# Performance work log

Measured on AMD Instinct MI355X. Metric: run time of the kernel, lower is better.

The kernel has to match this reference:

```python
import jax, jax.numpy as jnp
import numpy as np

B, T, C = 2, 2048, 2048
H, KH, D = 16, 4, 128
EPS = 1e-6

def _rmsnorm(x, w, eps=EPS):
    # norm over last dim in fp32, matching torch RMSNorm
    xf = x.astype(jnp.float32)
    var = jnp.mean(xf * xf, axis=-1, keepdims=True)
    return w * (xf * jax.lax.rsqrt(var + eps)).astype(x.dtype)

def _rotate_half(x):
    x1, x2 = jnp.split(x, 2, axis=-1)
    return jnp.concatenate((-x2, x1), axis=-1)

def setup_inputs() -> dict:
    key = jax.random.key(0)
    ks = jax.random.split(key, 9)
    s = 0.02
    return {
        "x": jax.random.normal(ks[0], (B, T, C), jnp.float32),
        "cos": jax.random.uniform(ks[1], (B, T, D), jnp.float32),
        "sin": jax.random.uniform(ks[2], (B, T, D), jnp.float32),
        "Wq": jax.random.normal(ks[3], (H * D, C), jnp.float32) * s,
        "Wk": jax.random.normal(ks[4], (KH * D, C), jnp.float32) * s,
        "Wv": jax.random.normal(ks[5], (KH * D, C), jnp.float32) * s,
        "Wo": jax.random.normal(ks[6], (C, H * D), jnp.float32) * s,
        "q_norm_w": jnp.ones((D,), jnp.float32),
        "k_norm_w": jnp.ones((D,), jnp.float32),
    }

def reference(x, cos, sin, Wq, Wk, Wv, Wo, q_norm_w, k_norm_w):
    rep = H // KH
    # projections (torch Linear: y = x @ W.T)
    q = jnp.einsum('btc,oc->bto', x, Wq).reshape(B, T, H, D)
    k = jnp.einsum('btc,oc->bto', x, Wk).reshape(B, T, KH, D)
    v = jnp.einsum('btc,oc->bto', x, Wv).reshape(B, T, KH, D)
    # per-head RMSNorm on d_head
    q = _rmsnorm(q, q_norm_w)
    k = _rmsnorm(k, k_norm_w)
    # RoPE, cos/sin broadcast over heads
    c = cos[:, :, None, :]
    s = sin[:, :, None, :]
    q = q * c + _rotate_half(q) * s
    k = k * c + _rotate_half(k) * s
    # GQA attention without materializing repeated k/v
    qg = q.reshape(B, T, KH, rep, D)
    scale = 1.0 / jnp.sqrt(jnp.asarray(D, jnp.float32))
    scores = jnp.einsum('bqhrd,bkhd->bhrqk', qg, k) * scale  # (B,KH,rep,T,T)
    causal = jnp.tril(jnp.ones((T, T), bool))
    scores = jnp.where(causal, scores, jnp.finfo(scores.dtype).min)
    attn = jax.nn.softmax(scores, axis=-1)
    y = jnp.einsum('bhrqk,bkhd->bqhrd', attn, v)  # (B,T,KH,rep,D)
    y = y.reshape(B, T, H * D)
    return jnp.einsum('bto,co->btc', y, Wo)
```

## Files before the change

kernel.cpp:

```cpp
#include <hip/hip_runtime.h>


typedef __attribute__((ext_vector_type(8))) short bf16x8;
typedef __attribute__((ext_vector_type(4))) float f32x4;
typedef __attribute__((ext_vector_type(16))) float f32x16;

__device__ __forceinline__ unsigned short f2bf(float f) {
  union { float f; unsigned u; } v; v.f = f;
  unsigned u = v.u;
  u += 0x7fffu + ((u >> 16) & 1u);
  return (unsigned short)(u >> 16);
}
__device__ __forceinline__ float bf2f(unsigned short h) {
  union { unsigned u; float f; } v; v.u = ((unsigned)h) << 16;
  return v.f;
}
__device__ __forceinline__ unsigned cvtpk_bf16(float lo, float hi) {
  unsigned r;
  asm("v_cvt_pk_bf16_f32 %0, %1, %2" : "=v"(r) : "v"(lo), "v"(hi));
  return r;
}

__device__ __forceinline__ void gl_lds16(const void* g, void* l) {
  __builtin_amdgcn_global_load_lds(
      (const __attribute__((address_space(1))) unsigned int*)(unsigned long long)g,
      (__attribute__((address_space(3))) unsigned int*)(unsigned int)(unsigned long long)l,
      16, 0, 0);
}

__global__ void cvt_all(const float* __restrict__ x, const float* __restrict__ wq,
                        const float* __restrict__ wk, const float* __restrict__ wv,
                        const float* __restrict__ wo,
                        unsigned short* __restrict__ xb,
                        unsigned short* __restrict__ wcat,
                        unsigned short* __restrict__ wob) {
  const long nx = 2097152, nq = 1048576, nk = 262144;
  const long b1 = nx, b2 = nx + nq, b3 = b2 + nk, b4 = b3 + nk;
  const long tot = b4 + 1048576;
  long i = (long)blockIdx.x * blockDim.x + threadIdx.x;
  const long stride = (long)gridDim.x * blockDim.x;
  for (; i < tot; i += stride) {
    float4 vv; unsigned short* dst; long o;
    if (i < b1)      { vv = ((const float4*)x)[i];       dst = xb;   o = i; }
    else if (i < b2) { vv = ((const float4*)wq)[i - b1]; dst = wcat; o = i - b1; }
    else if (i < b3) { vv = ((const float4*)wk)[i - b2]; dst = wcat; o = (i - b2) + nq; }
    else if (i < b4) { vv = ((const float4*)wv)[i - b3]; dst = wcat; o = (i - b3) + nq + nk; }
    else             { vv = ((const float4*)wo)[i - b4]; dst = wob;  o = i - b4; }
    ushort4 u;
    u.x = f2bf(vv.x); u.y = f2bf(vv.y); u.z = f2bf(vv.z); u.w = f2bf(vv.w);
    ((ushort4*)dst)[o] = u;
  }
}

#define PHASE(QM, QN, PF, GATE)                                               \
  {                                                                           \
    bf16x8 af[4][2], bg[2][2];                                                \
    _Pragma("unroll") for (int r = 0; r < 4; ++r) {                           \
      const char* pa = ldsc + curb + (((QM)*128 + arow0 + r*16) << 7);        \
      af[r][0] = *(const bf16x8*)(pa + csw0);                                 \
      af[r][1] = *(const bf16x8*)(pa + csw1);                                 \
    }                                                                         \
    _Pragma("unroll") for (int n = 0; n < 2; ++n) {                           \
      const char* pb = ldsc + curb + 32768 + (((QN)*128 + brow0 + n*16) << 7);\
      bg[n][0] = *(const bf16x8*)(pb + csw0);                                 \
      bg[n][1] = *(const bf16x8*)(pb + csw1);                                 \
    }                                                                         \
    PF                                                                        \
    __builtin_amdgcn_s_barrier();                                             \
    asm volatile("s_waitcnt lgkmcnt(0)" ::: "memory");                        \
    __builtin_amdgcn_sched_barrier(0);                                        \
    __builtin_amdgcn_s_setprio(1);                                            \
    _Pragma("unroll") for (int r = 0; r < 4; ++r)                             \
      _Pragma("unroll") for (int n = 0; n < 2; ++n) {                         \
        acc[(QM)*4+r][(QN)*2+n] = __builtin_amdgcn_mfma_f32_16x16x32_bf16(    \
            af[r][0], bg[n][0], acc[(QM)*4+r][(QN)*2+n], 0, 0, 0);            \
        acc[(QM)*4+r][(QN)*2+n] = __builtin_amdgcn_mfma_f32_16x16x32_bf16(    \
            af[r][1], bg[n][1], acc[(QM)*4+r][(QN)*2+n], 0, 0, 0);            \
      }                                                                       \
    __builtin_amdgcn_s_setprio(0);                                            \
    GATE                                                                      \
    __builtin_amdgcn_s_barrier();                                             \
  }

template <int OUT_BF16>
__global__ __launch_bounds__(512, 2)
void gemm256(const unsigned short* __restrict__ A,
             const unsigned short* __restrict__ Bm,
             void* __restrict__ Cp, int M, int N, int K) {
  __shared__ __align__(16) char ldsc[131072];
  const int nbn = N >> 8;
  int wg = blockIdx.x;
  {
    const int cpx = (int)gridDim.x >> 3;
    wg = (wg & 7) * cpx + (wg >> 3);
  }
  const int m0 = (wg / nbn) << 8, n0 = (wg % nbn) << 8;
  const int tid = threadIdx.x;
  const int lane = tid & 63, wid = tid >> 6;
  const int lr = lane & 15, lg = lane >> 4;
  const int wm = wid >> 2, wn = wid & 3;
  const int csw0 = (lg << 4) ^ ((lr & 7) << 4);
  const int csw1 = (64 + (lg << 4)) ^ ((lr & 7) << 4);
  const int arow0 = (wm << 6) + lr;
  const int brow0 = (wn << 5) + lr;
  const int srowL = tid >> 3;
  const int scol = ((tid & 7) ^ (srowL & 7)) << 3;
  const unsigned short* Asrc = A + (size_t)(m0 + srowL) * K + scol;
  const unsigned short* Bsrc = Bm + (size_t)(n0 + srowL) * K + scol;
  const int sdst = wid << 10;
  const int NT = K >> 6;
  f32x4 acc[8][4] = {};
  gl_lds16(Asrc, ldsc + sdst);
  gl_lds16(Asrc + (size_t)64 * K, ldsc + 8192 + sdst);
  gl_lds16(Bsrc, ldsc + 32768 + sdst);
  gl_lds16(Bsrc + (size_t)64 * K, ldsc + 40960 + sdst);
  gl_lds16(Asrc + (size_t)128 * K, ldsc + 16384 + sdst);
  gl_lds16(Asrc + (size_t)192 * K, ldsc + 24576 + sdst);
  gl_lds16(Bsrc + (size_t)128 * K, ldsc + 49152 + sdst);
  gl_lds16(Bsrc + (size_t)192 * K, ldsc + 57344 + sdst);
  asm volatile("s_waitcnt vmcnt(4)" ::: "memory");
  __builtin_amdgcn_s_barrier();

  for (int t = 0; t < NT; ++t) {
    const int curb = (t & 1) << 16;
    const int nxtb = curb ^ 65536;
    const size_t kn = (size_t)(t + 1) << 6;
    const bool pf = (t + 1) < NT;
    PHASE(0, 0,
      if (pf) { gl_lds16(Asrc + kn, ldsc + nxtb + sdst);
                gl_lds16(Asrc + (size_t)64 * K + kn, ldsc + nxtb + 8192 + sdst); },
      if (pf) { asm volatile("s_waitcnt vmcnt(2)" ::: "memory"); }
      else    { asm volatile("s_waitcnt vmcnt(0)" ::: "memory"); } )
    PHASE(1, 0,
      if (pf) { gl_lds16(Bsrc + kn, ldsc + nxtb + 32768 + sdst);
                gl_lds16(Bsrc + (size_t)64 * K + kn, ldsc + nxtb + 40960 + sdst); }, )
    PHASE(0, 1,
      if (pf) { gl_lds16(Asrc + (size_t)128 * K + kn, ldsc + nxtb + 16384 + sdst);
                gl_lds16(Asrc + (size_t)192 * K + kn, ldsc + nxtb + 24576 + sdst); }, )
    PHASE(1, 1,
      if (pf) { gl_lds16(Bsrc + (size_t)128 * K + kn, ldsc + nxtb + 49152 + sdst);
                gl_lds16(Bsrc + (size_t)192 * K + kn, ldsc + nxtb + 57344 + sdst); },
      if (pf) { asm volatile("s_waitcnt vmcnt(4)" ::: "memory"); } )
  }
  #pragma unroll
  for (int mi = 0; mi < 8; ++mi) {
    const int mrow = m0 + ((mi >> 2) << 7) + (wm << 6) + ((mi & 3) << 4) + (lg << 2);
    #pragma unroll
    for (int ni = 0; ni < 4; ++ni) {
      const int ncol = n0 + ((ni >> 1) << 7) + (wn << 5) + ((ni & 1) << 4) + lr;
      #pragma unroll
      for (int i = 0; i < 4; ++i) {
        if constexpr (OUT_BF16)
          ((unsigned short*)Cp)[(size_t)(mrow + i) * N + ncol] = f2bf(acc[mi][ni][i]);
        else
          ((float*)Cp)[(size_t)(mrow + i) * N + ncol] = acc[mi][ni][i];
      }
    }
  }
}

__global__ __launch_bounds__(512, 2)
void gemm128n(const unsigned short* __restrict__ A,
              const unsigned short* __restrict__ Bm,
              float* __restrict__ Cp, int M, int N, int K) {
  __shared__ __align__(16) char ldsc[98304];
  const int nbn = N >> 8;
  int wg = blockIdx.x;
  { const int cpx = (int)gridDim.x >> 3;
    wg = (wg & 7) * cpx + (wg >> 3); }
  const int m0 = (wg / nbn) << 7, n0 = (wg % nbn) << 8;
  const int tid = threadIdx.x;
  const int lane = tid & 63, wid = tid >> 6;
  const int lr = lane & 15, lg = lane >> 4;
  const int wm = wid >> 1, wn = wid & 1;
  const int csw0 = (lg << 4) ^ ((lr & 7) << 4);
  const int csw1 = (64 + (lg << 4)) ^ ((lr & 7) << 4);
  const int srowL = tid >> 3;
  const int scol = ((tid & 7) ^ (srowL & 7)) << 3;
  const unsigned short* Asrc = A + (size_t)(m0 + srowL) * K + scol;
  const unsigned short* Bsrc = Bm + (size_t)(n0 + srowL) * K + scol;
  const int sdst = wid << 10;
  const int NT = K >> 6;
  f32x4 acc[2][8] = {};
  gl_lds16(Asrc, ldsc + sdst);
  gl_lds16(Asrc + (size_t)64 * K, ldsc + 8192 + sdst);
  gl_lds16(Bsrc, ldsc + 16384 + sdst);
  gl_lds16(Bsrc + (size_t)128 * K, ldsc + 24576 + sdst);
  gl_lds16(Bsrc + (size_t)64 * K, ldsc + 32768 + sdst);
  gl_lds16(Bsrc + (size_t)192 * K, ldsc + 40960 + sdst);
  asm volatile("s_waitcnt vmcnt(2)" ::: "memory");
  __builtin_amdgcn_s_barrier();

  for (int t = 0; t < NT; ++t) {
    const int curb = (t & 1) ? 49152 : 0;
    const int nxtb = 49152 - curb;
    const size_t kn = (size_t)(t + 1) << 6;
    const bool pf = (t + 1) < NT;
    #pragma unroll
    for (int ph = 0; ph < 2; ++ph) {
      bf16x8 af[2][2], bg[4][2];
      #pragma unroll
      for (int r = 0; r < 2; ++r) {
        const char* pa = ldsc + curb + (((wm << 5) + (r << 4) + lr) << 7);
        af[r][0] = *(const bf16x8*)(pa + csw0);
        af[r][1] = *(const bf16x8*)(pa + csw1);
      }
      #pragma unroll
      for (int n = 0; n < 4; ++n) {
        const char* pb = ldsc + curb + 16384 + ((ph << 1) + wn) * 8192 +
                         (((n << 4) + lr) << 7);
        bg[n][0] = *(const bf16x8*)(pb + csw0);
        bg[n][1] = *(const bf16x8*)(pb + csw1);
      }
      if (pf) {
        if (ph == 0) {
          gl_lds16(Asrc + kn, ldsc + nxtb + sdst);
          gl_lds16(Asrc + (size_t)64 * K + kn, ldsc + nxtb + 8192 + sdst);
          gl_lds16(Bsrc + kn, ldsc + nxtb + 16384 + sdst);
          gl_lds16(Bsrc + (size_t)128 * K + kn, ldsc + nxtb + 24576 + sdst);
        } else {
          gl_lds16(Bsrc + (size_t)64 * K + kn, ldsc + nxtb + 32768 + sdst);
          gl_lds16(Bsrc + (size_t)192 * K + kn, ldsc + nxtb + 40960 + sdst);
        }
      }
      __builtin_amdgcn_s_barrier();
      asm volatile("s_waitcnt lgkmcnt(0)" ::: "memory");
      __builtin_amdgcn_sched_barrier(0);
      __builtin_amdgcn_s_setprio(1);
      #pragma unroll
      for (int r = 0; r < 2; ++r)
        #pragma unroll
        for (int n = 0; n < 4; ++n) {
          acc[r][ph * 4 + n] = __builtin_amdgcn_mfma_f32_16x16x32_bf16(
              af[r][0], bg[n][0], acc[r][ph * 4 + n], 0, 0, 0);
          acc[r][ph * 4 + n] = __builtin_amdgcn_mfma_f32_16x16x32_bf16(
              af[r][1], bg[n][1], acc[r][ph * 4 + n], 0, 0, 0);
        }
      __builtin_amdgcn_s_setprio(0);
      if (ph == 0) {
        if (pf) { asm volatile("s_waitcnt vmcnt(4)" ::: "memory"); }
        else    { asm volatile("s_waitcnt vmcnt(0)" ::: "memory"); }
      } else {
        if (pf) { asm volatile("s_waitcnt vmcnt(2)" ::: "memory"); }
      }
      __builtin_amdgcn_s_barrier();
    }
  }
  #pragma unroll
  for (int r = 0; r < 2; ++r) {
    const int mrow = m0 + (wm << 5) + (r << 4) + (lg << 2);
    #pragma unroll
    for (int n = 0; n < 8; ++n) {
      const int ncol = n0 + (wn << 7) + (n << 4) + lr;
      #pragma unroll
      for (int i = 0; i < 4; ++i)
        Cp[(size_t)(mrow + i) * N + ncol] = acc[r][n][i];
    }
  }
}

__global__ __launch_bounds__(256)
void norm_rope(const unsigned short* __restrict__ qkv,
               const float* __restrict__ cosb, const float* __restrict__ sinb,
               const float* __restrict__ qw, const float* __restrict__ kw,
               unsigned short* __restrict__ Qb,
               unsigned short* __restrict__ Kb) {
  const int wv = threadIdx.x >> 6, l = threadIdx.x & 63;
  const int rr = blockIdx.x * 4 + wv;
  const int hh = rr % 20, bt = rr / 20;
  const bool isq = hh < 16;
  const ushort2 u = *(const ushort2*)(qkv + (size_t)bt * 3072 + (hh << 7) + 2 * l);
  const float v0 = bf2f(u.x), v1 = bf2f(u.y);
  float ss = v0 * v0 + v1 * v1;
  #pragma unroll
  for (int off = 1; off < 64; off <<= 1) ss += __shfl_xor(ss, off);
  const float rms = rsqrtf(ss * (1.0f / 128.0f) + 1e-6f);
  const float* w = isq ? qw : kw;
  const float2 w2 = *(const float2*)(w + 2 * l);
  const float n0 = v0 * rms * w2.x, n1 = v1 * rms * w2.y;
  const float sx0 = __shfl_xor(n0, 32), sx1 = __shfl_xor(n1, 32);
  const float p0 = (l < 32) ? -sx0 : sx0;
  const float p1 = (l < 32) ? -sx1 : sx1;
  const float2 c2 = *(const float2*)(cosb + (size_t)bt * 128 + 2 * l);
  const float2 s2 = *(const float2*)(sinb + (size_t)bt * 128 + 2 * l);
  const float qsc = isq ? 0.08838834764831845f : 1.0f;
  ushort2 o;
  o.x = f2bf((n0 * c2.x + p0 * s2.x) * qsc);
  o.y = f2bf((n1 * c2.y + p1 * s2.y) * qsc);
  const int b = bt >> 11, t = bt & 2047;
  if (isq)
    *(ushort2*)(Qb + (((size_t)(b * 16 + hh) * 2048 + t) << 7) + 2 * l) = o;
  else
    *(ushort2*)(Kb + (((size_t)(b * 4 + (hh - 16)) * 2048 + t) << 7) + 2 * l) = o;
}

__global__ __launch_bounds__(256)
void v_trans(const unsigned short* __restrict__ qkv, unsigned short* __restrict__ Vt) {
  __shared__ unsigned short tile[64][68];
  const int b = blockIdx.x >> 2, h = blockIdx.x & 3;
  const int t0 = blockIdx.y << 6, d0 = blockIdx.z << 6;
  const int tid = threadIdx.x;
  #pragma unroll
  for (int p = 0; p < 4; ++p) {
    const int idx = ((p << 8) + tid) << 2;
    const int r = idx >> 6, c = idx & 63;
    *(ushort4*)(&tile[r][c]) = *(const ushort4*)(
        qkv + (size_t)(b * 2048 + t0 + r) * 3072 + 2560 + (h << 7) + d0 + c);
  }
  __syncthreads();
  unsigned short* vbase = Vt + (size_t)((b * 4 + h) * 128 + d0) * 2048 + t0;
  #pragma unroll
  for (int p = 0; p < 4; ++p) {
    const int idx = ((p << 8) + tid) << 2;
    const int d = idx >> 6, tq = idx & 63;
    const int tin = (tq & 48) | ((tq & 8) >> 1) | ((tq & 4) << 1);
    ushort4 u;
    u.x = tile[tin + 0][d];
    u.y = tile[tin + 1][d];
    u.z = tile[tin + 2][d];
    u.w = tile[tin + 3][d];
    *(ushort4*)(vbase + ((size_t)d << 11) + tq) = u;
  }
}

__global__ __launch_bounds__(512)
void attn_fwd(const unsigned short* __restrict__ Qb,
              const unsigned short* __restrict__ Kb,
              const unsigned short* __restrict__ Vt,
              unsigned short* __restrict__ Y) {
  __shared__ __align__(16) char L[65536];
  const int bh = blockIdx.x;
  const int b = bh >> 4, h = bh & 15, hk = h >> 2;
  const int py = blockIdx.y;
  const int p = (py < 8) ? py : 23 - py;
  const int tid = threadIdx.x;
  const int lane = tid & 63, wid = tid >> 6;
  const int g = wid >> 2;
  const int wid2 = wid & 3;
  const int j = wid2 >> 1;
  const int qt = (p << 1) + j;
  const int sub = (wid2 & 1) << 5;
  const int l31 = lane & 31, hi = lane >> 5;
  const int swb = (lane & 7) << 4;
  char* KsC = L + g * 32768;
  char* VsC = KsC + 16384;
  const unsigned short* Kp = Kb + (size_t)(b * 4 + hk) * 2048 * 128;
  const unsigned short* Vp = Vt + (size_t)(b * 4 + hk) * 128 * 2048;
  const int qg = qt * 64 + sub + l31;
  const unsigned short* Qp = Qb + (size_t)((b * 16 + h) * 2048 + qg) * 128;
  bf16x8 aq[8];
  #pragma unroll
  for (int ks = 0; ks < 8; ++ks)
    aq[ks] = *(const bf16x8*)(Qp + (ks << 4) + (hi << 3));
  float m_i = -1e30f, l_i = 0.f;
  f32x16 acc[4] = {};
  const int kr_in = (lane >> 4), kcb = (lane & 15) << 4;
  const int vr_in = (lane >> 3), vcb = (lane & 7) << 4;
  const int nkb = (p << 1) + 2;
  const int nit = (nkb + 1) >> 1;

  for (int it = 0; it < nit; ++it) {
    const int kb = 2 * it + g;
    const bool act = kb < nkb;
    if (act) {
      const int k0 = kb << 6;
      #pragma unroll
      for (int i = 0; i < 4; ++i) {
        const int c = (wid2 << 2) + i;
        { const int r = (c << 2) + kr_in;
          const int sw = kcb ^ ((r & 7) << 4);
          gl_lds16(Kp + (size_t)(k0 + r) * 128 + (sw >> 1), KsC + (c << 10)); }
        { const int r = (c << 3) + vr_in;
          const int sw = vcb ^ ((r & 7) << 4);
          gl_lds16(Vp + (size_t)r * 2048 + k0 + (sw >> 1), VsC + (c << 10)); }
      }
    }
    __syncthreads();
    if (act && kb <= qt) {
      const int k0 = kb << 6;
      f32x16 s[2] = {};
      __builtin_amdgcn_s_setprio(1);
      #pragma unroll
      for (int sblk = 0; sblk < 2; ++sblk) {
        const int row = (sblk << 5) + l31;
        #pragma unroll
        for (int ks = 0; ks < 8; ++ks) {
          const bf16x8 bk = *(const bf16x8*)(
              KsC + (row << 8) + (((ks << 5) + (hi << 4)) ^ swb));
          s[sblk] = __builtin_amdgcn_mfma_f32_32x32x16_bf16(bk, aq[ks], s[sblk], 0, 0, 0);
        }
      }
      __builtin_amdgcn_s_setprio(0);
      if (kb == qt) {
        #pragma unroll
        for (int sblk = 0; sblk < 2; ++sblk)
          #pragma unroll
          for (int r = 0; r < 16; ++r) {
            const int kv = k0 + (sblk << 5) + (r & 3) + ((r >> 2) << 3) + (hi << 2);
            if (kv > qg) s[sblk][r] = -1e30f;
          }
      }
      float mx = s[0][0];
      #pragma unroll
      for (int sblk = 0; sblk < 2; ++sblk)
        #pragma unroll
        for (int r = 0; r < 16; ++r) mx = fmaxf(mx, s[sblk][r]);
      mx = fmaxf(mx, __shfl_xor(mx, 32));
      if (!__all(mx <= m_i + 8.0f)) {
        const float mn = fmaxf(m_i, mx);
        const float r = __expf(m_i - mn);
        m_i = mn;
        l_i *= r;
        #pragma unroll
        for (int d = 0; d < 4; ++d)
          #pragma unroll
          for (int i = 0; i < 16; ++i) acc[d][i] *= r;
      }
      float se = 0.f;
      unsigned pk[16];
      #pragma unroll
      for (int t2 = 0; t2 < 16; ++t2) {
        const int f0 = 2 * t2, f1 = 2 * t2 + 1;
        const float e0 = __expf(s[f0 >> 4][f0 & 15] - m_i);
        const float e1 = __expf(s[f1 >> 4][f1 & 15] - m_i);
        se += e0 + e1;
        pk[t2] = cvtpk_bf16(e0, e1);
      }
      se += __shfl_xor(se, 32);
      l_i += se;
      __builtin_amdgcn_s_setprio(1);
      #pragma unroll
      for (int dblk = 0; dblk < 4; ++dblk) {
        const int row = (dblk << 5) + l31;
        #pragma unroll
        for (int cp = 0; cp < 4; ++cp) {
          const bf16x8 va = *(const bf16x8*)(
              VsC + (row << 7) + (((cp << 5) + (hi << 4)) ^ swb));
          union { unsigned u[4]; bf16x8 v; } pb;
          pb.u[0] = pk[cp * 4 + 0]; pb.u[1] = pk[cp * 4 + 1];
          pb.u[2] = pk[cp * 4 + 2]; pb.u[3] = pk[cp * 4 + 3];
          acc[dblk] = __builtin_amdgcn_mfma_f32_32x32x16_bf16(va, pb.v, acc[dblk], 0, 0, 0);
        }
      }
      __builtin_amdgcn_s_setprio(0);
    }
    __syncthreads();
  }

  float* cb = (float*)L;
  #pragma unroll
  for (int jj = 0; jj < 2; ++jj) {
    const int base = (((wid2 & 1) << 6) + lane) * 66;
    if (g == 1 && j == jj) {
      #pragma unroll
      for (int d = 0; d < 4; ++d)
        #pragma unroll
        for (int i = 0; i < 16; ++i) cb[base + d * 16 + i] = acc[d][i];
      cb[base + 64] = m_i;
      cb[base + 65] = l_i;
    }
    __syncthreads();
    if (g == 0 && j == jj) {
      const float m1 = cb[base + 64], l1v = cb[base + 65];
      const float m = fmaxf(m_i, m1);
      const float e0 = __expf(m_i - m), e1 = __expf(m1 - m);
      const float inv = 1.0f / (l_i * e0 + l1v * e1);
      unsigned short* Yp = Y + (((size_t)b * 2048 + qg) * 16 + h) * 128;
      #pragma unroll
      for (int dblk = 0; dblk < 4; ++dblk) {
        #pragma unroll
        for (int qd = 0; qd < 4; ++qd) {
          ushort4 o;
          o.x = f2bf((acc[dblk][qd * 4 + 0] * e0 + cb[base + dblk * 16 + qd * 4 + 0] * e1) * inv);
          o.y = f2bf((acc[dblk][qd * 4 + 1] * e0 + cb[base + dblk * 16 + qd * 4 + 1] * e1) * inv);
          o.z = f2bf((acc[dblk][qd * 4 + 2] * e0 + cb[base + dblk * 16 + qd * 4 + 2] * e1) * inv);
          o.w = f2bf((acc[dblk][qd * 4 + 3] * e0 + cb[base + dblk * 16 + qd * 4 + 3] * e1) * inv);
          *(ushort4*)(Yp + (dblk << 5) + (qd << 3) + (hi << 2)) = o;
        }
      }
    }
    __syncthreads();
  }
}

extern "C" void kernel_launch(void* const* d_in, const int* in_sizes, int n_in,
                              void* d_out, int out_size, void* d_ws, size_t ws_size,
                              hipStream_t stream) {
  const float* x    = (const float*)d_in[0];
  const float* cosb = (const float*)d_in[1];
  const float* sinb = (const float*)d_in[2];
  const float* Wq   = (const float*)d_in[3];
  const float* Wk   = (const float*)d_in[4];
  const float* Wv   = (const float*)d_in[5];
  const float* Wo   = (const float*)d_in[6];
  const float* qw   = (const float*)d_in[7];
  const float* kw   = (const float*)d_in[8];
  char* ws = (char*)d_ws;
  unsigned short* xb   = (unsigned short*)(ws);
  unsigned short* Wcat = (unsigned short*)(ws + (16ull << 20));
  unsigned short* Wob  = (unsigned short*)(ws + (28ull << 20));
  unsigned short* qkv  = (unsigned short*)(ws + (36ull << 20));
  unsigned short* Qb   = (unsigned short*)(ws + (60ull << 20));
  unsigned short* Kb   = (unsigned short*)(ws + (76ull << 20));
  unsigned short* Vt   = (unsigned short*)(ws + (80ull << 20));

  cvt_all<<<2048, 256, 0, stream>>>(x, Wq, Wk, Wv, Wo, xb, Wcat, Wob);

  gemm256<1><<<192, 512, 0, stream>>>(xb, Wcat, qkv, 4096, 3072, 2048);
  norm_rope<<<2 * 2048 * 20 / 4, 256, 0, stream>>>(qkv, cosb, sinb, qw, kw, Qb, Kb);
  v_trans<<<dim3(8, 32, 2), 256, 0, stream>>>(qkv, Vt);
  attn_fwd<<<dim3(32, 16), 512, 0, stream>>>(Qb, Kb, Vt, xb);
  gemm128n<<<256, 512, 0, stream>>>(xb, Wob, (float*)d_out, 4096, 2048, 2048);
}
```

Measured before the change: 207.7 us.

## Retile QKV projection GEMM to 128x384 tiles for full CU coverage

Replaces the 256x256-tile QKV GEMM (192 workgroups) with a 128x384-tile kernel launched on 256 workgroups, so the grid fills all compute units on MI355X instead of leaving some idle. The LDS layout, prefetch schedule and vmcnt waits are reworked for the new A/B split, with each warp computing a 32x48 subtile per phase. Each tile now has lower arithmetic intensity and more B traffic per FLOP. The bespoke wait counts add a risk of ordering mistakes.

```diff
diff --git a/kernel.cpp b/kernel.cpp
--- a/kernel.cpp
+++ b/kernel.cpp
@@ -52,16 +52,17 @@
   }
 }
 
-#define PHASE(QM, QN, PF, GATE)                                               \
+#define PH384(QM, QN, PF, GATE)                                               \
   {                                                                           \
-    bf16x8 af[4][2], bg[2][2];                                                \
-    _Pragma("unroll") for (int r = 0; r < 4; ++r) {                           \
-      const char* pa = ldsc + curb + (((QM)*128 + arow0 + r*16) << 7);        \
+    bf16x8 af[2][2], bg[3][2];                                                \
+    _Pragma("unroll") for (int r = 0; r < 2; ++r) {                           \
+      const char* pa = ldsc + curb + (((QM)*64 + (wm << 5) + r*16 + lr) << 7);\
       af[r][0] = *(const bf16x8*)(pa + csw0);                                 \
       af[r][1] = *(const bf16x8*)(pa + csw1);                                 \
     }                                                                         \
-    _Pragma("unroll") for (int n = 0; n < 2; ++n) {                           \
-      const char* pb = ldsc + curb + 32768 + (((QN)*128 + brow0 + n*16) << 7);\
+    _Pragma("unroll") for (int n = 0; n < 3; ++n) {                           \
+      const char* pb = ldsc + curb + 16384 +                                  \
+                       (((QN)*192 + wn*48 + n*16 + lr) << 7);                 \
       bg[n][0] = *(const bf16x8*)(pb + csw0);                                 \
       bg[n][1] = *(const bf16x8*)(pb + csw1);                                 \
     }                                                                         \
@@ -70,54 +71,51 @@
     asm volatile("s_waitcnt lgkmcnt(0)" ::: "memory");                        \
     __builtin_amdgcn_sched_barrier(0);                                        \
     __builtin_amdgcn_s_setprio(1);                                            \
-    _Pragma("unroll") for (int r = 0; r < 4; ++r)                             \
-      _Pragma("unroll") for (int n = 0; n < 2; ++n) {                         \
-        acc[(QM)*4+r][(QN)*2+n] = __builtin_amdgcn_mfma_f32_16x16x32_bf16(    \
-            af[r][0], bg[n][0], acc[(QM)*4+r][(QN)*2+n], 0, 0, 0);            \
-        acc[(QM)*4+r][(QN)*2+n] = __builtin_amdgcn_mfma_f32_16x16x32_bf16(    \
-            af[r][1], bg[n][1], acc[(QM)*4+r][(QN)*2+n], 0, 0, 0);            \
+    _Pragma("unroll") for (int r = 0; r < 2; ++r)                             \
+      _Pragma("unroll") for (int n = 0; n < 3; ++n) {                         \
+        acc[(QM)*2+r][(QN)*3+n] = __builtin_amdgcn_mfma_f32_16x16x32_bf16(    \
+            af[r][0], bg[n][0], acc[(QM)*2+r][(QN)*3+n], 0, 0, 0);            \
+        acc[(QM)*2+r][(QN)*3+n] = __builtin_amdgcn_mfma_f32_16x16x32_bf16(    \
+            af[r][1], bg[n][1], acc[(QM)*2+r][(QN)*3+n], 0, 0, 0);            \
       }                                                                       \
     __builtin_amdgcn_s_setprio(0);                                            \
     GATE                                                                      \
     __builtin_amdgcn_s_barrier();                                             \
   }
 
-template <int OUT_BF16>
 __global__ __launch_bounds__(512, 2)
-void gemm256(const unsigned short* __restrict__ A,
+void gemm384(const unsigned short* __restrict__ A,
              const unsigned short* __restrict__ Bm,
-             void* __restrict__ Cp, int M, int N, int K) {
+             unsigned short* __restrict__ Cp, int M, int N, int K) {
   __shared__ __align__(16) char ldsc[131072];
-  const int nbn = N >> 8;
+  const int nbn = N / 384;
   int wg = blockIdx.x;
   {
     const int cpx = (int)gridDim.x >> 3;
     wg = (wg & 7) * cpx + (wg >> 3);
   }
-  const int m0 = (wg / nbn) << 8, n0 = (wg % nbn) << 8;
+  const int m0 = (wg / nbn) << 7, n0 = (wg % nbn) * 384;
   const int tid = threadIdx.x;
   const int lane = tid & 63, wid = tid >> 6;
   const int lr = lane & 15, lg = lane >> 4;
   const int wm = wid >> 2, wn = wid & 3;
   const int csw0 = (lg << 4) ^ ((lr & 7) << 4);
   const int csw1 = (64 + (lg << 4)) ^ ((lr & 7) << 4);
-  const int arow0 = (wm << 6) + lr;
-  const int brow0 = (wn << 5) + lr;
   const int srowL = tid >> 3;
   const int scol = ((tid & 7) ^ (srowL & 7)) << 3;
   const unsigned short* Asrc = A + (size_t)(m0 + srowL) * K + scol;
   const unsigned short* Bsrc = Bm + (size_t)(n0 + srowL) * K + scol;
   const int sdst = wid << 10;
   const int NT = K >> 6;
-  f32x4 acc[8][4] = {};
+  f32x4 acc[4][6] = {};
   gl_lds16(Asrc, ldsc + sdst);
+  gl_lds16(Bsrc, ldsc + 16384 + sdst);
+  gl_lds16(Bsrc + (size_t)64 * K, ldsc + 24576 + sdst);
+  gl_lds16(Bsrc + (size_t)128 * K, ldsc + 32768 + sdst);
   gl_lds16(Asrc + (size_t)64 * K, ldsc + 8192 + sdst);
-  gl_lds16(Bsrc, ldsc + 32768 + sdst);
-  gl_lds16(Bsrc + (size_t)64 * K, ldsc + 40960 + sdst);
-  gl_lds16(Asrc + (size_t)128 * K, ldsc + 16384 + sdst);
-  gl_lds16(Asrc + (size_t)192 * K, ldsc + 24576 + sdst);
-  gl_lds16(Bsrc + (size_t)128 * K, ldsc + 49152 + sdst);
-  gl_lds16(Bsrc + (size_t)192 * K, ldsc + 57344 + sdst);
+  gl_lds16(Bsrc + (size_t)192 * K, ldsc + 40960 + sdst);
+  gl_lds16(Bsrc + (size_t)256 * K, ldsc + 49152 + sdst);
+  gl_lds16(Bsrc + (size_t)320 * K, ldsc + 57344 + sdst);
   asm volatile("s_waitcnt vmcnt(4)" ::: "memory");
   __builtin_amdgcn_s_barrier();
 
@@ -126,35 +124,33 @@
     const int nxtb = curb ^ 65536;
     const size_t kn = (size_t)(t + 1) << 6;
     const bool pf = (t + 1) < NT;
-    PHASE(0, 0,
+    PH384(0, 0,
       if (pf) { gl_lds16(Asrc + kn, ldsc + nxtb + sdst);
-                gl_lds16(Asrc + (size_t)64 * K + kn, ldsc + nxtb + 8192 + sdst); },
-      if (pf) { asm volatile("s_waitcnt vmcnt(2)" ::: "memory"); }
+                gl_lds16(Bsrc + kn, ldsc + nxtb + 16384 + sdst); },
+      if (pf) { asm volatile("s_waitcnt vmcnt(5)" ::: "memory"); }
+      else    { asm volatile("s_waitcnt vmcnt(3)" ::: "memory"); } )
+    PH384(1, 0,
+      if (pf) { gl_lds16(Bsrc + (size_t)64 * K + kn, ldsc + nxtb + 24576 + sdst);
+                gl_lds16(Bsrc + (size_t)128 * K + kn, ldsc + nxtb + 32768 + sdst); },
+      if (pf) { asm volatile("s_waitcnt vmcnt(4)" ::: "memory"); }
       else    { asm volatile("s_waitcnt vmcnt(0)" ::: "memory"); } )
-    PHASE(1, 0,
-      if (pf) { gl_lds16(Bsrc + kn, ldsc + nxtb + 32768 + sdst);
-                gl_lds16(Bsrc + (size_t)64 * K + kn, ldsc + nxtb + 40960 + sdst); }, )
-    PHASE(0, 1,
-      if (pf) { gl_lds16(Asrc + (size_t)128 * K + kn, ldsc + nxtb + 16384 + sdst);
-                gl_lds16(Asrc + (size_t)192 * K + kn, ldsc + nxtb + 24576 + sdst); }, )
-    PHASE(1, 1,
-      if (pf) { gl_lds16(Bsrc + (size_t)128 * K + kn, ldsc + nxtb + 49152 + sdst);
-                gl_lds16(Bsrc + (size_t)192 * K + kn, ldsc + nxtb + 57344 + sdst); },
+    PH384(0, 1,
+      if (pf) { gl_lds16(Asrc + (size_t)64 * K + kn, ldsc + nxtb + 8192 + sdst);
+                gl_lds16(Bsrc + (size_t)192 * K + kn, ldsc + nxtb + 40960 + sdst); }, )
+    PH384(1, 1,
+      if (pf) { gl_lds16(Bsrc + (size_t)256 * K + kn, ldsc + nxtb + 49152 + sdst);
+                gl_lds16(Bsrc + (size_t)320 * K + kn, ldsc + nxtb + 57344 + sdst); },
       if (pf) { asm volatile("s_waitcnt vmcnt(4)" ::: "memory"); } )
   }
   #pragma unroll
-  for (int mi = 0; mi < 8; ++mi) {
-    const int mrow = m0 + ((mi >> 2) << 7) + (wm << 6) + ((mi & 3) << 4) + (lg << 2);
+  for (int mi = 0; mi < 4; ++mi) {
+    const int mrow = m0 + ((mi >> 1) << 6) + (wm << 5) + ((mi & 1) << 4) + (lg << 2);
     #pragma unroll
-    for (int ni = 0; ni < 4; ++ni) {
-      const int ncol = n0 + ((ni >> 1) << 7) + (wn << 5) + ((ni & 1) << 4) + lr;
-      #pragma unroll
-      for (int i = 0; i < 4; ++i) {
-        if constexpr (OUT_BF16)
-          ((unsigned short*)Cp)[(size_t)(mrow + i) * N + ncol] = f2bf(acc[mi][ni][i]);
-        else
-          ((float*)Cp)[(size_t)(mrow + i) * N + ncol] = acc[mi][ni][i];
-      }
+    for (int ni = 0; ni < 6; ++ni) {
+      const int ncol = n0 + (ni >= 3 ? 192 : 0) + wn * 48 + (ni % 3) * 16 + lr;
+      #pragma unroll
+      for (int i = 0; i < 4; ++i)
+        Cp[(size_t)(mrow + i) * N + ncol] = f2bf(acc[mi][ni][i]);
     }
   }
 }
@@ -506,7 +502,7 @@
 
   cvt_all<<<2048, 256, 0, stream>>>(x, Wq, Wk, Wv, Wo, xb, Wcat, Wob);
 
-  gemm256<1><<<192, 512, 0, stream>>>(xb, Wcat, qkv, 4096, 3072, 2048);
+  gemm384<<<256, 512, 0, stream>>>(xb, Wcat, qkv, 4096, 3072, 2048);
   norm_rope<<<2 * 2048 * 20 / 4, 256, 0, stream>>>(qkv, cosb, sinb, qw, kw, Qb, Kb);
   v_trans<<<dim3(8, 32, 2), 256, 0, stream>>>(qkv, Vt);
   attn_fwd<<<dim3(32, 16), 512, 0, stream>>>(Qb, Kb, Vt, xb);
```

Result: faster. 199.2 us (-4.1%).
